# Performance work log

Measured on AMD Instinct MI355X. Metric: run time of the kernel, lower is better.

The kernel has to match this reference:

```python
import jax, jax.numpy as jnp
import numpy as np

D_MODEL = 1024
NHEAD = 16
DIM_HEAD = 64
SCALE = DIM_HEAD ** (-0.5)


def setup_inputs() -> dict:
    key = jax.random.key(0)
    ks = jax.random.split(key, 8)
    B, N = 2, 2048
    inner = NHEAD * DIM_HEAD
    s = 0.02
    return {
        "query": jax.random.normal(ks[0], (B, N, D_MODEL), jnp.float32),
        "key": jax.random.normal(ks[1], (B, N, D_MODEL), jnp.float32),
        "value": jax.random.normal(ks[2], (B, N, D_MODEL), jnp.float32),
        "Wq": jax.random.normal(ks[3], (D_MODEL, inner), jnp.float32) * s,
        "Wk": jax.random.normal(ks[4], (D_MODEL, inner), jnp.float32) * s,
        "Wv": jax.random.normal(ks[5], (D_MODEL, inner), jnp.float32) * s,
        "Wo": jax.random.normal(ks[6], (inner, D_MODEL), jnp.float32) * s,
        "bo": jnp.zeros((D_MODEL,), jnp.float32),
    }


def reference(query, key, value, Wq, Wk, Wv, Wo, bo):
    B, Nq, _ = query.shape
    Nk = key.shape[1]
    # projections (no bias), split heads: [B, N, h, d]
    q = (query @ Wq).reshape(B, Nq, NHEAD, DIM_HEAD)
    k = (key @ Wk).reshape(B, Nk, NHEAD, DIM_HEAD)
    v = (value @ Wv).reshape(B, Nk, NHEAD, DIM_HEAD)
    # scores [B, h, Nq, Nk]
    sim = jnp.einsum('bihd,bjhd->bhij', q, k) * SCALE
    attn = jax.nn.softmax(sim, axis=-1)  # dropout p=0.0 -> identity
    out = jnp.einsum('bhij,bjhd->bihd', attn, v).reshape(B, Nq, NHEAD * DIM_HEAD)
    return out @ Wo + bo
```

## Files before the change

kernel.cpp:

```cpp
#include <hip/hip_runtime.h>
#include <stdint.h>

typedef __attribute__((ext_vector_type(8))) short short8;
typedef __attribute__((ext_vector_type(8))) unsigned short ushort8;
typedef __attribute__((ext_vector_type(4))) unsigned short ushort4v;
typedef __attribute__((ext_vector_type(4))) float float4v;

#define D_MODEL 1024
#define NHEAD 16
#define DIM_HEAD 64
#define BATCH 2
#define SEQ 2048
#define BH (BATCH*NHEAD)
#define MROWS (BATCH*SEQ)
#define MK ((size_t)MROWS * D_MODEL)

__device__ __forceinline__ unsigned short f2bf(float f) {
  union { float f; unsigned u; } v; v.f = f;
  unsigned r = v.u + 0x7fffu + ((v.u >> 16) & 1u);
  return (unsigned short)(r >> 16);
}
__device__ __forceinline__ unsigned short f2bf_fast(float f) {
  union { float f; unsigned u; } v; v.f = f;
  return (unsigned short)((v.u + 0x8000u) >> 16);
}

__device__ __forceinline__ float fexp2(float x) {
#if __has_builtin(__builtin_amdgcn_exp2f)
  return __builtin_amdgcn_exp2f(x);
#else
  return exp2f(x);
#endif
}

__device__ __forceinline__ void gld16(const unsigned short* g, unsigned short* l) {
  __builtin_amdgcn_global_load_lds(
      (const __attribute__((address_space(1))) unsigned int*)g,
      (__attribute__((address_space(3))) unsigned int*)l, 16, 0, 0);
}

__global__ __launch_bounds__(256) void wtrans_kernel(const float* __restrict__ W0,
    const float* __restrict__ W1, const float* __restrict__ W2,
    const float* __restrict__ W3, unsigned short* __restrict__ WT) {
  __shared__ float tile[32][33];
  const int z = blockIdx.z;
  const float* W = (z == 0) ? W0 : (z == 1) ? W1 : (z == 2) ? W2 : W3;
  const float scale = (z == 0) ? 0.18033688f : 1.0f;
  unsigned short* dst = WT + ((size_t)z << 20);
  int bn = blockIdx.x * 32;
  int bk = blockIdx.y * 32;
  int tx = threadIdx.x & 31, ty = threadIdx.x >> 5;
#pragma unroll
  for (int i = 0; i < 4; i++)
    tile[ty + i*8][tx] = W[(size_t)(bk + ty + i*8) * D_MODEL + bn + tx];
  __syncthreads();
#pragma unroll
  for (int i = 0; i < 4; i++)
    dst[(size_t)(bn + ty + i*8) * D_MODEL + bk + tx] = f2bf(tile[tx][ty + i*8] * scale);
}

__global__ __launch_bounds__(256) void cast_kernel(const float* __restrict__ q,
    const float* __restrict__ k, const float* __restrict__ v,
    unsigned short* __restrict__ out) {
  const float* src = (blockIdx.y == 0) ? q : (blockIdx.y == 1) ? k : v;
  unsigned short* dst = out + (size_t)blockIdx.y * MK;
  size_t idx = ((size_t)blockIdx.x * 256 + threadIdx.x) * 8;
  float4v a = *(const float4v*)(src + idx);
  float4v b = *(const float4v*)(src + idx + 4);
  ushort8 o;
  o[0] = f2bf(a[0]); o[1] = f2bf(a[1]); o[2] = f2bf(a[2]); o[3] = f2bf(a[3]);
  o[4] = f2bf(b[0]); o[5] = f2bf(b[1]); o[6] = f2bf(b[2]); o[7] = f2bf(b[3]);
  *(ushort8*)(dst + idx) = o;
}

__global__ __launch_bounds__(256) void vtrans_kernel(const unsigned short* __restrict__ Vb,
                                                     unsigned short* __restrict__ VT) {
  __shared__ unsigned short tile[64][72];
  const int bh = blockIdx.x;
  const int b = bh >> 4, h = bh & 15;
  const int n0 = blockIdx.y * 64;
  const int t = threadIdx.x;
#pragma unroll
  for (int p = 0; p < 2; p++) {
    int g = p*256 + t; int row = g >> 3, c = g & 7;
    *(ushort8*)&tile[row][c*8] =
      *(const ushort8*)(Vb + ((size_t)((b*SEQ + n0 + row)*NHEAD + h))*DIM_HEAD + c*8);
  }
  __syncthreads();
  int d = t >> 2, base = (t & 3) * 16;
  ushort8 o0, o1;
#pragma unroll
  for (int m = 0; m < 8; m++) {
    int e0 = base + m, e1 = base + 8 + m;
    int k0_ = 32*(e0>>5) + 16*((e0>>2)&1) + 4*((e0>>3)&3) + (e0&3);
    int k1_ = 32*(e1>>5) + 16*((e1>>2)&1) + 4*((e1>>3)&3) + (e1&3);
    o0[m] = tile[k0_][d];
    o1[m] = tile[k1_][d];
  }
  unsigned short* dst = VT + ((size_t)(bh*DIM_HEAD + d))*SEQ + n0 + base;
  *(ushort8*)dst = o0;
  *(ushort8*)(dst + 8) = o1;
}

__global__ __launch_bounds__(256, 3) void proj_kernel(const unsigned short* __restrict__ Xbf,
    const unsigned short* __restrict__ WT0, unsigned short* __restrict__ Y0) {
  __shared__ unsigned short Al[128*64];
  __shared__ unsigned short Bl[128*64];
  const int z = blockIdx.z;
  const unsigned short* A  = Xbf + (size_t)z * MK;
  const unsigned short* BT = WT0 + ((size_t)z << 20);
  unsigned short* Y = Y0 + (size_t)z * MK;
  const int m0 = blockIdx.x * 128, n0 = blockIdx.y * 128;
  const int t = threadIdx.x;
  const int lane = t & 63, w = t >> 6, quad = lane >> 4, lid = lane & 15;
  const int wm = w & 1, wn = w >> 1;
  const int r8 = lane >> 3, c8 = (lane & 7) * 8;

  float4v acc[4][4];
#pragma unroll
  for (int i = 0; i < 4; i++)
#pragma unroll
    for (int j = 0; j < 4; j++) acc[i][j] = (float4v)0.0f;

  for (int k0 = 0; k0 < D_MODEL; k0 += 64) {
#pragma unroll
    for (int p = 0; p < 4; p++) {
      int seg = w*4 + p;
      gld16(A  + (size_t)(m0 + seg*8 + r8) * D_MODEL + k0 + c8, &Al[seg*8*64]);
      gld16(BT + (size_t)(n0 + seg*8 + r8) * D_MODEL + k0 + c8, &Bl[seg*8*64]);
    }
    __syncthreads();
#pragma unroll
    for (int kst = 0; kst < 2; kst++) {
      short8 af[4], bfr[4];
#pragma unroll
      for (int i = 0; i < 4; i++)
        af[i] = *(const short8*)&Al[(wm*64 + i*16 + lid)*64 + kst*32 + quad*8];
#pragma unroll
      for (int j = 0; j < 4; j++)
        bfr[j] = *(const short8*)&Bl[(wn*64 + j*16 + lid)*64 + kst*32 + quad*8];
#pragma unroll
      for (int i = 0; i < 4; i++)
#pragma unroll
        for (int j = 0; j < 4; j++)
          acc[i][j] = __builtin_amdgcn_mfma_f32_16x16x32_bf16(af[i], bfr[j], acc[i][j], 0, 0, 0);
    }
    __syncthreads();
  }
#pragma unroll
  for (int i = 0; i < 4; i++)
#pragma unroll
    for (int j = 0; j < 4; j++)
#pragma unroll
      for (int r = 0; r < 4; r++) {
        int row = m0 + wm*64 + i*16 + quad*4 + r;
        int col = n0 + wn*64 + j*16 + lid;
        Y[(size_t)row * D_MODEL + col] = f2bf_fast(acc[i][j][r]);
      }
}

__global__ __launch_bounds__(256, 3) void outproj_kernel(const unsigned short* __restrict__ A,
    const unsigned short* __restrict__ WT, const float* __restrict__ bias,
    float* __restrict__ out) {
  __shared__ unsigned short Al[64*64];
  __shared__ unsigned short Bl[128*64];
  const int m0 = blockIdx.x * 64, n0 = blockIdx.y * 128;
  const int t = threadIdx.x;
  const int lane = t & 63, w = t >> 6, quad = lane >> 4, lid = lane & 15;
  const int wm = w & 1, wn = w >> 1;
  const int r8 = lane >> 3, c8 = (lane & 7) * 8;

  float4v acc[2][4];
#pragma unroll
  for (int i = 0; i < 2; i++)
#pragma unroll
    for (int j = 0; j < 4; j++) acc[i][j] = (float4v)0.0f;

  for (int k0 = 0; k0 < D_MODEL; k0 += 64) {
#pragma unroll
    for (int p = 0; p < 2; p++) {
      int seg = w*2 + p;
      gld16(A + (size_t)(m0 + seg*8 + r8) * D_MODEL + k0 + c8, &Al[seg*8*64]);
    }
#pragma unroll
    for (int p = 0; p < 4; p++) {
      int seg = w*4 + p;
      gld16(WT + (size_t)(n0 + seg*8 + r8) * D_MODEL + k0 + c8, &Bl[seg*8*64]);
    }
    __syncthreads();
#pragma unroll
    for (int kst = 0; kst < 2; kst++) {
      short8 af[2], bfr[4];
#pragma unroll
      for (int i = 0; i < 2; i++)
        af[i] = *(const short8*)&Al[(wm*32 + i*16 + lid)*64 + kst*32 + quad*8];
#pragma unroll
      for (int j = 0; j < 4; j++)
        bfr[j] = *(const short8*)&Bl[(wn*64 + j*16 + lid)*64 + kst*32 + quad*8];
#pragma unroll
      for (int i = 0; i < 2; i++)
#pragma unroll
        for (int j = 0; j < 4; j++)
          acc[i][j] = __builtin_amdgcn_mfma_f32_16x16x32_bf16(af[i], bfr[j], acc[i][j], 0, 0, 0);
    }
    __syncthreads();
  }
#pragma unroll
  for (int i = 0; i < 2; i++)
#pragma unroll
    for (int j = 0; j < 4; j++)
#pragma unroll
      for (int r = 0; r < 4; r++) {
        int row = m0 + wm*32 + i*16 + quad*4 + r;
        int col = n0 + wn*64 + j*16 + lid;
        out[(size_t)row * D_MODEL + col] = acc[i][j][r] + bias[col];
      }
}

#define QB 128
#define KB 64
#define FSTR 72
#define NT (SEQ/KB)

__global__ __launch_bounds__(256, 2) void flash_kernel(const unsigned short* __restrict__ Q,
    const unsigned short* __restrict__ K, const unsigned short* __restrict__ VT,
    unsigned short* __restrict__ O) {
  __shared__ unsigned short Kl[2][KB][FSTR];
  __shared__ unsigned short Vt[2][DIM_HEAD][FSTR];

  const int bh = blockIdx.x;
  const int b = bh >> 4, h = bh & 15;
  const int q0 = blockIdx.y * QB;
  const int t = threadIdx.x;
  const int lane = t & 63, w = t >> 6, quad = lane >> 4, lid = lane & 15;
  const int prow = t >> 3, pc = (t & 7) * 8;

  const unsigned short* Kbase = K + ((size_t)(b*SEQ)*NHEAD + h)*DIM_HEAD;
  const unsigned short* Vbase = VT + (size_t)bh*DIM_HEAD*SEQ;

  short8 qf[2][2];
#pragma unroll
  for (int st = 0; st < 2; st++)
#pragma unroll
    for (int kst = 0; kst < 2; kst++)
      qf[st][kst] = *(const short8*)(Q +
          ((size_t)((b*SEQ + q0 + w*32 + st*16 + lid)*NHEAD + h))*DIM_HEAD + kst*32 + quad*8);

  float4v o[2][4];
#pragma unroll
  for (int st = 0; st < 2; st++)
#pragma unroll
    for (int i = 0; i < 4; i++) o[st][i] = (float4v)0.0f;
  float ps[2] = {0.0f, 0.0f};

  auto LOADT = [&](int kb, ushort8* kr, ushort8* vr) {
#pragma unroll
    for (int p = 0; p < 2; p++) {
      int row = p*32 + prow;
      kr[p] = *(const ushort8*)(Kbase + (size_t)(kb + row) * D_MODEL + pc);
      vr[p] = *(const ushort8*)(Vbase + (size_t)row * SEQ + kb + pc);
    }
  };
  auto COMMIT = [&](int bi, const ushort8* kr, const ushort8* vr) {
#pragma unroll
    for (int p = 0; p < 2; p++) {
      int row = p*32 + prow;
      *(ushort8*)&Kl[bi][row][pc] = kr[p];
      *(ushort8*)&Vt[bi][row][pc] = vr[p];
    }
  };
  auto STEP = [&](int bi) {
    float4v s[2][4];
#pragma unroll
    for (int st = 0; st < 2; st++)
#pragma unroll
      for (int n = 0; n < 4; n++) s[st][n] = (float4v)0.0f;
    __builtin_amdgcn_s_setprio(1);
#pragma unroll
    for (int kst = 0; kst < 2; kst++)
#pragma unroll
      for (int n = 0; n < 4; n++) {
        short8 kf = *(const short8*)&Kl[bi][n*16 + lid][kst*32 + quad*8];
        s[0][n] = __builtin_amdgcn_mfma_f32_16x16x32_bf16(kf, qf[0][kst], s[0][n], 0, 0, 0);
        s[1][n] = __builtin_amdgcn_mfma_f32_16x16x32_bf16(kf, qf[1][kst], s[1][n], 0, 0, 0);
      }
    __builtin_amdgcn_s_setprio(0);
    union PF { unsigned u[4]; short8 v8; };
    PF pf0[2], pf1[2];
#pragma unroll
    for (int n = 0; n < 4; n++) {
      float p0[4], p1[4];
#pragma unroll
      for (int r = 0; r < 4; r++) {
        p0[r] = fexp2(s[0][n][r]);
        p1[r] = fexp2(s[1][n][r]);
        ps[0] += p0[r]; ps[1] += p1[r];
      }
      const int hh = n >> 1, bb = 2*(n & 1);
      asm("v_cvt_pk_bf16_f32 %0, %1, %2" : "=v"(pf0[hh].u[bb+0]) : "v"(p0[0]), "v"(p0[1]));
      asm("v_cvt_pk_bf16_f32 %0, %1, %2" : "=v"(pf0[hh].u[bb+1]) : "v"(p0[2]), "v"(p0[3]));
      asm("v_cvt_pk_bf16_f32 %0, %1, %2" : "=v"(pf1[hh].u[bb+0]) : "v"(p1[0]), "v"(p1[1]));
      asm("v_cvt_pk_bf16_f32 %0, %1, %2" : "=v"(pf1[hh].u[bb+1]) : "v"(p1[2]), "v"(p1[3]));
    }
    __builtin_amdgcn_s_setprio(1);
#pragma unroll
    for (int kst = 0; kst < 2; kst++)
#pragma unroll
      for (int i = 0; i < 4; i++) {
        short8 vf = *(const short8*)&Vt[bi][i*16 + lid][kst*32 + quad*8];
        o[0][i] = __builtin_amdgcn_mfma_f32_16x16x32_bf16(pf0[kst].v8, vf, o[0][i], 0, 0, 0);
        o[1][i] = __builtin_amdgcn_mfma_f32_16x16x32_bf16(pf1[kst].v8, vf, o[1][i], 0, 0, 0);
      }
    __builtin_amdgcn_s_setprio(0);
  };

  ushort8 krA[2], vrA[2], krB[2], vrB[2];
  LOADT(0, krA, vrA);
  LOADT(KB, krB, vrB);
  COMMIT(0, krA, vrA);
  __syncthreads();

  for (int i = 0; i < NT; i += 2) {
    if (i + 2 < NT) LOADT((i + 2)*KB, krA, vrA);
    STEP(0);
    if (i + 1 < NT) COMMIT(1, krB, vrB);
    __syncthreads();
    if (i + 3 < NT) LOADT((i + 3)*KB, krB, vrB);
    STEP(1);
    if (i + 2 < NT) COMMIT(0, krA, vrA);
    __syncthreads();
  }

  float dr[2][4];
#pragma unroll
  for (int st = 0; st < 2; st++) {
    float v = ps[st];
    v += __shfl_xor(v, 16);
    v += __shfl_xor(v, 32);
    v = 1.0f / v;
#pragma unroll
    for (int r = 0; r < 4; r++) dr[st][r] = __shfl(v, quad*4 + r);
  }
#pragma unroll
  for (int st = 0; st < 2; st++)
#pragma unroll
    for (int i = 0; i < 4; i++)
#pragma unroll
      for (int r = 0; r < 4; r++) {
        int q = q0 + w*32 + st*16 + quad*4 + r;
        O[((size_t)((b*SEQ + q)*NHEAD + h))*DIM_HEAD + i*16 + lid] =
          f2bf(o[st][i][r] * dr[st][r]);
      }
}

extern "C" void kernel_launch(void* const* d_in, const int* in_sizes, int n_in,
                              void* d_out, int out_size, void* d_ws, size_t ws_size,
                              hipStream_t stream) {
  const float* query = (const float*)d_in[0];
  const float* key_  = (const float*)d_in[1];
  const float* value = (const float*)d_in[2];
  const float* Wq = (const float*)d_in[3];
  const float* Wk = (const float*)d_in[4];
  const float* Wv = (const float*)d_in[5];
  const float* Wo = (const float*)d_in[6];
  const float* bo = (const float*)d_in[7];
  float* out = (float*)d_out;

  char* ws = (char*)d_ws;
  unsigned short* WqT = (unsigned short*)(ws + (0ll  << 20));
  unsigned short* WoT = (unsigned short*)(ws + (6ll  << 20));
  unsigned short* Xbf = (unsigned short*)(ws + (8ll  << 20));
  unsigned short* Qb  = (unsigned short*)(ws + (32ll << 20));
  unsigned short* Kb  = Qb + MK;
  unsigned short* Vb  = Qb + 2*MK;
  unsigned short* VT  = (unsigned short*)(ws + (8ll  << 20));
  unsigned short* Ob  = (unsigned short*)(ws + (16ll << 20));

  dim3 tb(256);
  dim3 tg(32, 32, 4);
  hipLaunchKernelGGL(wtrans_kernel, tg, tb, 0, stream, Wq, Wk, Wv, Wo, WqT);

  dim3 cg(MK / (256*8), 3);
  hipLaunchKernelGGL(cast_kernel, cg, tb, 0, stream, query, key_, value, Xbf);

  dim3 pg(MROWS/128, D_MODEL/128, 3);
  hipLaunchKernelGGL(proj_kernel, pg, tb, 0, stream, Xbf, WqT, Qb);

  dim3 vg(BH, SEQ/64);
  hipLaunchKernelGGL(vtrans_kernel, vg, tb, 0, stream, Vb, VT);

  dim3 fg(BH, SEQ/QB);
  hipLaunchKernelGGL(flash_kernel, fg, tb, 0, stream, Qb, Kb, VT, Ob);

  dim3 og(MROWS/64, D_MODEL/128);
  hipLaunchKernelGGL(outproj_kernel, og, tb, 0, stream, Ob, WoT, bo, out);
}
```

Before: 210.8 us.

## Fuse weight transpose with input cast and write V transposed from projection epilogue

Merges the weight-transpose and fp32-to-bf16 input cast into one prep kernel. Each transpose block now handles two tiles, so the two jobs fit one launch grid. The V projection epilogue writes its output directly in the permuted, transposed layout the flash kernel expects, which removes the separate vtrans kernel and its extra read and write of V. The cost is scattered 8-byte stores in the V epilogue in place of the contiguous row stores, and the prep kernel reserves shared memory for the cast blocks even though they do not use it.

```diff
diff --git a/kernel.cpp b/kernel.cpp
--- a/kernel.cpp
+++ b/kernel.cpp
@@ -39,67 +39,44 @@
       (__attribute__((address_space(3))) unsigned int*)l, 16, 0, 0);
 }
 
-__global__ __launch_bounds__(256) void wtrans_kernel(const float* __restrict__ W0,
-    const float* __restrict__ W1, const float* __restrict__ W2,
-    const float* __restrict__ W3, unsigned short* __restrict__ WT) {
+__global__ __launch_bounds__(256) void prep_kernel(const float* __restrict__ q,
+    const float* __restrict__ k, const float* __restrict__ v,
+    unsigned short* __restrict__ Xbf,
+    const float* __restrict__ W0, const float* __restrict__ W1,
+    const float* __restrict__ W2, const float* __restrict__ W3,
+    unsigned short* __restrict__ WT) {
+  if (blockIdx.y < 3) {
+    const float* src = (blockIdx.y == 0) ? q : (blockIdx.y == 1) ? k : v;
+    unsigned short* dst = Xbf + (size_t)blockIdx.y * MK;
+    size_t idx = ((size_t)blockIdx.x * 256 + threadIdx.x) * 8;
+    float4v a = *(const float4v*)(src + idx);
+    float4v b = *(const float4v*)(src + idx + 4);
+    ushort8 o;
+    o[0] = f2bf(a[0]); o[1] = f2bf(a[1]); o[2] = f2bf(a[2]); o[3] = f2bf(a[3]);
+    o[4] = f2bf(b[0]); o[5] = f2bf(b[1]); o[6] = f2bf(b[2]); o[7] = f2bf(b[3]);
+    *(ushort8*)(dst + idx) = o;
+    return;
+  }
   __shared__ float tile[32][33];
-  const int z = blockIdx.z;
+  const int z = blockIdx.x >> 9;
   const float* W = (z == 0) ? W0 : (z == 1) ? W1 : (z == 2) ? W2 : W3;
   const float scale = (z == 0) ? 0.18033688f : 1.0f;
   unsigned short* dst = WT + ((size_t)z << 20);
-  int bn = blockIdx.x * 32;
-  int bk = blockIdx.y * 32;
   int tx = threadIdx.x & 31, ty = threadIdx.x >> 5;
 #pragma unroll
-  for (int i = 0; i < 4; i++)
-    tile[ty + i*8][tx] = W[(size_t)(bk + ty + i*8) * D_MODEL + bn + tx];
-  __syncthreads();
-#pragma unroll
-  for (int i = 0; i < 4; i++)
-    dst[(size_t)(bn + ty + i*8) * D_MODEL + bk + tx] = f2bf(tile[tx][ty + i*8] * scale);
-}
-
-__global__ __launch_bounds__(256) void cast_kernel(const float* __restrict__ q,
-    const float* __restrict__ k, const float* __restrict__ v,
-    unsigned short* __restrict__ out) {
-  const float* src = (blockIdx.y == 0) ? q : (blockIdx.y == 1) ? k : v;
-  unsigned short* dst = out + (size_t)blockIdx.y * MK;
-  size_t idx = ((size_t)blockIdx.x * 256 + threadIdx.x) * 8;
-  float4v a = *(const float4v*)(src + idx);
-  float4v b = *(const float4v*)(src + idx + 4);
-  ushort8 o;
-  o[0] = f2bf(a[0]); o[1] = f2bf(a[1]); o[2] = f2bf(a[2]); o[3] = f2bf(a[3]);
-  o[4] = f2bf(b[0]); o[5] = f2bf(b[1]); o[6] = f2bf(b[2]); o[7] = f2bf(b[3]);
-  *(ushort8*)(dst + idx) = o;
-}
-
-__global__ __launch_bounds__(256) void vtrans_kernel(const unsigned short* __restrict__ Vb,
-                                                     unsigned short* __restrict__ VT) {
-  __shared__ unsigned short tile[64][72];
-  const int bh = blockIdx.x;
-  const int b = bh >> 4, h = bh & 15;
-  const int n0 = blockIdx.y * 64;
-  const int t = threadIdx.x;
-#pragma unroll
-  for (int p = 0; p < 2; p++) {
-    int g = p*256 + t; int row = g >> 3, c = g & 7;
-    *(ushort8*)&tile[row][c*8] =
-      *(const ushort8*)(Vb + ((size_t)((b*SEQ + n0 + row)*NHEAD + h))*DIM_HEAD + c*8);
-  }
-  __syncthreads();
-  int d = t >> 2, base = (t & 3) * 16;
-  ushort8 o0, o1;
-#pragma unroll
-  for (int m = 0; m < 8; m++) {
-    int e0 = base + m, e1 = base + 8 + m;
-    int k0_ = 32*(e0>>5) + 16*((e0>>2)&1) + 4*((e0>>3)&3) + (e0&3);
-    int k1_ = 32*(e1>>5) + 16*((e1>>2)&1) + 4*((e1>>3)&3) + (e1&3);
-    o0[m] = tile[k0_][d];
-    o1[m] = tile[k1_][d];
-  }
-  unsigned short* dst = VT + ((size_t)(bh*DIM_HEAD + d))*SEQ + n0 + base;
-  *(ushort8*)dst = o0;
-  *(ushort8*)(dst + 8) = o1;
+  for (int rep = 0; rep < 2; rep++) {
+    int tl = (blockIdx.x & 511) * 2 + rep;
+    int bn = (tl & 31) * 32;
+    int bk = (tl >> 5) * 32;
+#pragma unroll
+    for (int i = 0; i < 4; i++)
+      tile[ty + i*8][tx] = W[(size_t)(bk + ty + i*8) * D_MODEL + bn + tx];
+    __syncthreads();
+#pragma unroll
+    for (int i = 0; i < 4; i++)
+      dst[(size_t)(bn + ty + i*8) * D_MODEL + bk + tx] = f2bf(tile[tx][ty + i*8] * scale);
+    __syncthreads();
+  }
 }
 
 __global__ __launch_bounds__(256, 3) void proj_kernel(const unsigned short* __restrict__ Xbf,
@@ -147,6 +124,26 @@
     }
     __syncthreads();
   }
+  if (z == 2) {
+#pragma unroll
+    for (int i = 0; i < 4; i++) {
+      int row = m0 + wm*64 + i*16 + quad*4;
+      int b_ = row >> 11;
+      int n_ = row & 2047;
+      int nblk = n_ & ~63;
+      int ebase = ((i >> 1) << 5) | (quad << 3) | ((i & 1) << 2);
+#pragma unroll
+      for (int j = 0; j < 4; j++) {
+        int col = n0 + wn*64 + j*16 + lid;
+        ushort4v pk;
+#pragma unroll
+        for (int r = 0; r < 4; r++) pk[r] = f2bf_fast(acc[i][j][r]);
+        *(ushort4v*)(Y + ((size_t)((b_*NHEAD + (col >> 6))*DIM_HEAD + (col & 63)))*SEQ
+                       + nblk + ebase) = pk;
+      }
+    }
+    return;
+  }
 #pragma unroll
   for (int i = 0; i < 4; i++)
 #pragma unroll
@@ -372,23 +369,17 @@
   unsigned short* Xbf = (unsigned short*)(ws + (8ll  << 20));
   unsigned short* Qb  = (unsigned short*)(ws + (32ll << 20));
   unsigned short* Kb  = Qb + MK;
-  unsigned short* Vb  = Qb + 2*MK;
-  unsigned short* VT  = (unsigned short*)(ws + (8ll  << 20));
+  unsigned short* VT  = Qb + 2*MK;
   unsigned short* Ob  = (unsigned short*)(ws + (16ll << 20));
 
   dim3 tb(256);
-  dim3 tg(32, 32, 4);
-  hipLaunchKernelGGL(wtrans_kernel, tg, tb, 0, stream, Wq, Wk, Wv, Wo, WqT);
-
-  dim3 cg(MK / (256*8), 3);
-  hipLaunchKernelGGL(cast_kernel, cg, tb, 0, stream, query, key_, value, Xbf);
+  dim3 pr(2048, 4);
+  hipLaunchKernelGGL(prep_kernel, pr, tb, 0, stream,
+                     query, key_, value, Xbf, Wq, Wk, Wv, Wo, WqT);
 
   dim3 pg(MROWS/128, D_MODEL/128, 3);
   hipLaunchKernelGGL(proj_kernel, pg, tb, 0, stream, Xbf, WqT, Qb);
 
-  dim3 vg(BH, SEQ/64);
-  hipLaunchKernelGGL(vtrans_kernel, vg, tb, 0, stream, Vb, VT);
-
   dim3 fg(BH, SEQ/QB);
   hipLaunchKernelGGL(flash_kernel, fg, tb, 0, stream, Qb, Kb, VT, Ob);
 
```

New measurement: 205.4 us, median of 2. 2.6% less time.
